# Kernel optimization log

Measured on AMD Instinct MI355X. Metric: run time of the kernel, lower is better.

The kernel has to match this reference:

```python
import jax, jax.numpy as jnp
import numpy as np

I, H, M, C, LOC, K = 512, 256, 80, 1024, 32, 31
C2 = C // 2
B, S, T = 32, 256, 800


def setup_inputs() -> dict:
    key = jax.random.key(0)
    ks = jax.random.split(key, 20)
    sc = 0.02
    return {
        "encodings": jax.random.normal(ks[0], (B, S, I), jnp.float32),
        "queries": jax.random.normal(ks[1], (B, T, H), jnp.float32),
        "outputs": jax.random.normal(ks[2], (B, T, M), jnp.float32),
        "mask": jnp.ones((B, S), jnp.float32),
        # GRUCell (PyTorch layout: gates ordered r, z, n)
        "w_ih": jax.random.normal(ks[3], (3 * C, I + H), jnp.float32) * sc,
        "w_hh": jax.random.normal(ks[4], (3 * C, C), jnp.float32) * sc,
        "b_ih": jax.random.normal(ks[5], (3 * C,), jnp.float32) * sc,
        "b_hh": jax.random.normal(ks[6], (3 * C,), jnp.float32) * sc,
        "w_q": jax.random.normal(ks[7], (C2, C), jnp.float32) * sc,        # proj_query
        "w_loc1": jax.random.normal(ks[8], (LOC, 1, K), jnp.float32) * sc, # Conv1d(1, loc, K)
        "w_loc2": jax.random.normal(ks[9], (C2, LOC), jnp.float32) * sc,   # Conv1d(loc, C2, 1)
        "w_k": jax.random.normal(ks[10], (C2, I), jnp.float32) * sc,       # proj_key
        "b_k": jax.random.normal(ks[11], (C2,), jnp.float32) * sc,
        "w_agg": jax.random.normal(ks[12], (C2,), jnp.float32) * sc,       # Conv1d(C2, 1, 1)
        "w_t1": jax.random.normal(ks[13], (C, I + C + M), jnp.float32) * sc,
        "b_t1": jax.random.normal(ks[14], (C,), jnp.float32) * sc,
        "w_t2": jax.random.normal(ks[15], (C,), jnp.float32) * sc,
    }


def _conv1d(x, w, pad):
    # x: [B, Cin, S], w: [Cout, Cin, K]
    return jax.lax.conv_general_dilated(
        x, w, window_strides=(1,), padding=[(pad, pad)],
        dimension_numbers=("NCH", "OIH", "NCH"))


def _aligner(encodings, queries, outputs, maskb,
             w_ih, w_hh, b_ih, b_hh, w_q, w_loc1, w_loc2, w_k, b_k,
             w_agg, w_t1, b_t1, w_t2):
    bsize, seqlen, _ = encodings.shape
    # key projection: [B, S, C2]
    key = encodings @ w_k.T + b_k
    h0 = jnp.zeros((bsize, C), encodings.dtype)
    align0 = jnp.full((bsize, seqlen), 1.0 / seqlen, encodings.dtype)
    alpha0 = jnp.zeros((bsize, seqlen), encodings.dtype).at[:, 0].set(1.0)
    trans0 = jnp.full((bsize, 1), 0.5, encodings.dtype)

    def step(carry, xt):
        h, align, trans, alpha = carry
        query, frame = xt  # [B,H], [B,M]
        prev = jnp.einsum("bsi,bs->bi", encodings, alpha)
        x = jnp.concatenate([query, prev], axis=-1)  # [B, H+I]
        gx = x @ w_ih.T + b_ih
        gh = h @ w_hh.T + b_hh
        xr, xz, xn = jnp.split(gx, 3, axis=-1)
        hr, hz, hn = jnp.split(gh, 3, axis=-1)
        r = jax.nn.sigmoid(xr + hr)
        z = jax.nn.sigmoid(xz + hz)
        n = jnp.tanh(xn + r * hn)
        h_new = (1.0 - z) * n + z * h  # GRUCell update
        # location features: [B,1,S] -> [B,LOC,S] -> [B,C2,S]
        loc = _conv1d(align[:, None, :], w_loc1, K // 2)
        loc = jnp.einsum("cl,bls->bcs", w_loc2, loc)
        score = loc + (h_new @ w_q.T)[..., None] + key.swapaxes(1, 2)  # [B,C2,S]
        energy = jnp.einsum("c,bcs->bs", w_agg, jnp.tanh(score))
        energy = jnp.where(maskb, -jnp.inf, energy)
        align_new = jax.nn.softmax(energy, axis=-1)
        shifted = jnp.pad(alpha, ((0, 0), (1, 0)))[:, :-1]  # F.pad(alpha, [1,-1])
        alpha_new = ((1.0 - trans) * alpha + trans * shifted + 1e-7) * align_new
        alpha_new = alpha_new / alpha_new.sum(axis=-1, keepdims=True)
        attend = jnp.einsum("bsi,bs->bi", encodings, alpha_new)
        t_in = jnp.concatenate([attend, frame, h_new], axis=-1)
        t = jax.nn.sigmoid(jnp.tanh(t_in @ w_t1.T + b_t1) @ w_t2[:, None])  # [B,1]
        return (h_new, align_new, t, alpha_new), alpha_new

    xs = (queries.swapaxes(0, 1), outputs.swapaxes(0, 1))
    _, alphas = jax.lax.scan(step, (h0, align0, trans0, alpha0), xs)
    return alphas.swapaxes(0, 1)  # [B, T, S]


def reference(encodings, queries, outputs, mask,
              w_ih, w_hh, b_ih, b_hh, w_q, w_loc1, w_loc2, w_k, b_k,
              w_agg, w_t1, b_t1, w_t2):
    maskb = ~(mask.astype(bool))
    return _aligner(encodings, queries, outputs, maskb,
                    w_ih, w_hh, b_ih, b_hh, w_q, w_loc1, w_loc2, w_k, b_k,
                    w_agg, w_t1, b_t1, w_t2)
```

## Files before the change

kernel.cpp:

```cpp
#include <hip/hip_runtime.h>
#include <cstdint>
#include <cstddef>


namespace cfg {
constexpr int NB = 32, NS = 256, NI = 512, NHq = 256, NM = 80;
constexpr int NC = 1024, NC2 = 512, NT = 800;
constexpr int NBLK = 256, NTHR = 512;

constexpr size_t OFF_KEYT  = 0;
constexpr size_t OFF_WKT   = OFF_KEYT + (size_t)NB * NS * NC2;
constexpr size_t OFF_PU    = OFF_WKT + (size_t)NI * NC2;
constexpr size_t OFF_H     = OFF_PU + (size_t)2 * NB * NI;
constexpr size_t OFF_H16   = OFF_H + (size_t)2 * NC * NB;
constexpr size_t OFF_E     = OFF_H16 + (size_t)NB * NC;
constexpr size_t OFF_W     = OFF_E + (size_t)2 * NB * NS;
constexpr size_t OFF_SE    = OFF_W + (size_t)2 * NB * NS;
constexpr size_t OFF_SW    = OFF_SE + 64;
constexpr size_t OFF_TPART = OFF_SW + 64;
constexpr size_t OFF_TRED  = OFF_TPART + (size_t)NBLK * NB;
constexpr size_t OFF_QBUF  = OFF_TRED + 32;
constexpr size_t OFF_BAR   = OFF_QBUF + (size_t)NB * NC2;
constexpr size_t OFF_Q16   = OFF_BAR + 4608;
constexpr size_t OFF_F16   = OFF_Q16 + (size_t)NT * NB * NHq / 2;
constexpr size_t OFF_WQ16  = OFF_F16 + (size_t)NT * NB * 128 / 2;
constexpr size_t WS_FLOATS = OFF_WQ16 + (size_t)NC2 * NC / 2;
}
using namespace cfg;

typedef __attribute__((ext_vector_type(8))) short short8;
typedef __attribute__((ext_vector_type(4))) float f32x4;

#define MF(a, b, c) __builtin_amdgcn_mfma_f32_16x16x32_bf16((a), (b), (c), 0, 0, 0)
#define LDSC(d, p) asm volatile("global_load_dwordx4 %0, %1, off sc0 sc1" : "=v"(d) : "v"(p))

__device__ __forceinline__ float ld_cg(const float* p) {
  return __hip_atomic_load(p, __ATOMIC_RELAXED, __HIP_MEMORY_SCOPE_AGENT);
}
__device__ __forceinline__ void st_cg(float* p, float v) {
  __hip_atomic_store(p, v, __ATOMIC_RELAXED, __HIP_MEMORY_SCOPE_AGENT);
}
__device__ __forceinline__ void st_cg_u16(unsigned short* p, unsigned short v) {
  asm volatile("global_store_short %0, %1, off sc0 sc1" :: "v"(p), "v"((unsigned)v) : "memory");
}

__device__ __forceinline__ void vw7(short8& a0, short8& a1, short8& a2, short8& a3,
                                    short8& a4, short8& a5, short8& a6) {
  asm volatile("s_waitcnt vmcnt(0)"
               : "+v"(a0), "+v"(a1), "+v"(a2), "+v"(a3), "+v"(a4), "+v"(a5), "+v"(a6));
}
__device__ __forceinline__ void vw8(short8& a0, short8& a1, short8& a2, short8& a3,
                                    short8& a4, short8& a5, short8& a6, short8& a7) {
  asm volatile("s_waitcnt vmcnt(0)"
               : "+v"(a0), "+v"(a1), "+v"(a2), "+v"(a3), "+v"(a4), "+v"(a5), "+v"(a6), "+v"(a7));
}
__device__ __forceinline__ void vw10(short8& a0, short8& a1, short8& a2, short8& a3, short8& a4,
                                     short8& a5, short8& a6, short8& a7, short8& a8, short8& a9) {
  asm volatile("s_waitcnt vmcnt(0)"
               : "+v"(a0), "+v"(a1), "+v"(a2), "+v"(a3), "+v"(a4), "+v"(a5), "+v"(a6),
                 "+v"(a7), "+v"(a8), "+v"(a9));
}
__device__ __forceinline__ void vw15(short8& a0, short8& a1, short8& a2, short8& a3, short8& a4,
                                     short8& a5, short8& a6, short8& a7, short8& a8, short8& a9,
                                     short8& aa, short8& ab2, short8& ac, short8& ad, short8& ae) {
  asm volatile("s_waitcnt vmcnt(0)"
               : "+v"(a0), "+v"(a1), "+v"(a2), "+v"(a3), "+v"(a4), "+v"(a5), "+v"(a6),
                 "+v"(a7), "+v"(a8), "+v"(a9), "+v"(aa), "+v"(ab2), "+v"(ac), "+v"(ad), "+v"(ae));
}
__device__ __forceinline__ void vw16f(f32x4& a0, f32x4& a1, f32x4& a2, f32x4& a3, f32x4& a4,
                                      f32x4& a5, f32x4& a6, f32x4& a7, f32x4& b0, f32x4& b1,
                                      f32x4& b2, f32x4& b3, f32x4& b4, f32x4& b5, f32x4& b6,
                                      f32x4& b7) {
  asm volatile("s_waitcnt vmcnt(0)"
               : "+v"(a0), "+v"(a1), "+v"(a2), "+v"(a3), "+v"(a4), "+v"(a5), "+v"(a6), "+v"(a7),
                 "+v"(b0), "+v"(b1), "+v"(b2), "+v"(b3), "+v"(b4), "+v"(b5), "+v"(b6), "+v"(b7));
}

__device__ __forceinline__ float frcp(float x) {
#if __has_builtin(__builtin_amdgcn_rcpf)
  return __builtin_amdgcn_rcpf(x);
#else
  return 1.f / x;
#endif
}
__device__ __forceinline__ float fsig(float x) { return frcp(1.f + __expf(-x)); }
__device__ __forceinline__ float ftanh(float x) {
  const float e = __expf(2.f * x);
  return 1.f - 2.f * frcp(e + 1.f);
}
__device__ __forceinline__ short f2bf(float f) {
  unsigned u = __float_as_uint(f);
  u += 0x7FFFu + ((u >> 16) & 1u);
  return (short)(u >> 16);
}
__device__ __forceinline__ float bf2f(short s) {
  return __uint_as_float(((unsigned)(unsigned short)s) << 16);
}
__device__ __forceinline__ short8 cvt8(f32x4 lo, f32x4 hi) {
  short8 a;
  a[0] = f2bf(lo[0]); a[1] = f2bf(lo[1]); a[2] = f2bf(lo[2]); a[3] = f2bf(lo[3]);
  a[4] = f2bf(hi[0]); a[5] = f2bf(hi[1]); a[6] = f2bf(hi[2]); a[7] = f2bf(hi[3]);
  return a;
}

__device__ __forceinline__ void gbarrier(unsigned* root, unsigned* flags, unsigned& ph) {
  ++ph;
  asm volatile("s_waitcnt vmcnt(0)" ::: "memory");
  __syncthreads();
  if (blockIdx.x == 0) {
    const int t = threadIdx.x;
    if (t > 0 && t < 256) {
      while (__hip_atomic_load(&flags[t * 16], __ATOMIC_RELAXED, __HIP_MEMORY_SCOPE_AGENT) < ph)
        __builtin_amdgcn_s_sleep(1);
    }
    __syncthreads();
    if (t == 0)
      __hip_atomic_store(root, ph, __ATOMIC_RELAXED, __HIP_MEMORY_SCOPE_AGENT);
  } else {
    if (threadIdx.x == 0) {
      __hip_atomic_store(&flags[blockIdx.x * 16], ph, __ATOMIC_RELAXED, __HIP_MEMORY_SCOPE_AGENT);
      while (__hip_atomic_load(root, __ATOMIC_RELAXED, __HIP_MEMORY_SCOPE_AGENT) < ph)
        __builtin_amdgcn_s_sleep(1);
    }
  }
  __syncthreads();
}

__device__ __forceinline__ float wcat_val(const float* __restrict__ w_ih,
                                          const float* __restrict__ w_hh,
                                          const float* __restrict__ w_t1,
                                          int kind, int c, int k) {
  if (kind < 3) {
    const int gr = kind * NC + c;
    if (k < 768) return w_ih[(size_t)gr * 768 + k];
    if (k < 1792) return w_hh[(size_t)gr * NC + (k - 768)];
    return 0.f;
  }
  if (k >= 256 && k < 768) return w_t1[(size_t)c * 1616 + (k - 256)];
  if (k >= 768 && k < 1792) return w_t1[(size_t)c * 1616 + 592 + (k - 768)];
  if (k >= 1792 && k < 1872) return w_t1[(size_t)c * 1616 + 512 + (k - 1792)];
  return 0.f;
}

__global__ void k_init(const float* __restrict__ enc, const float* __restrict__ queries,
                       const float* __restrict__ outputs, const float* __restrict__ w_k,
                       const float* __restrict__ w_q, float* __restrict__ ws) {
  const size_t t0 = (size_t)blockIdx.x * blockDim.x + threadIdx.x;
  const size_t gs = (size_t)gridDim.x * blockDim.x;
  for (size_t x = t0; x < (size_t)NI * NC2; x += gs) {
    const int i = (int)(x / NC2), c2 = (int)(x % NC2);
    ws[OFF_WKT + x] = w_k[(size_t)c2 * NI + i];
  }
  for (size_t x = t0; x < (size_t)NB * NI; x += gs) {
    const int b = (int)(x / NI), i = (int)(x % NI);
    ws[OFF_PU + x] = 0.f;
    ws[OFF_PU + (size_t)NB * NI + b * NI + i] = enc[(size_t)b * NS * NI + i];
  }
  for (size_t x = t0; x < (size_t)2 * NC * NB; x += gs) ws[OFF_H + x] = 0.f;
  for (size_t x = t0; x < (size_t)NB * NC; x += gs) ws[OFF_H16 + x] = 0.f;
  for (size_t x = t0; x < (size_t)NB * NS; x += gs) {
    ws[OFF_E + x] = 0.f;
    ws[OFF_E + (size_t)NB * NS + x] = 1.f;
    ws[OFF_W + x] = 0.f;
    ws[OFF_W + (size_t)NB * NS + x] = ((x & (NS - 1)) == 0) ? 1.f : 0.f;
  }
  for (size_t x = t0; x < (size_t)NB; x += gs) {
    ws[OFF_SE + x] = 0.f; ws[OFF_SE + NB + x] = (float)NS;
    ws[OFF_SW + x] = 0.f; ws[OFF_SW + NB + x] = 1.f;
    ws[OFF_TRED + x] = 0.f;
  }
  unsigned* bar = (unsigned*)(ws + OFF_BAR);
  for (size_t x = t0; x < 4608; x += gs) bar[x] = 0u;
  unsigned short* Q16 = (unsigned short*)(ws + OFF_Q16);
  for (size_t x = t0; x < (size_t)NT * NB * NHq; x += gs) {
    const int k = (int)(x & (NHq - 1));
    const int b = (int)((x >> 8) & (NB - 1));
    const int t = (int)(x >> 13);
    Q16[x] = (unsigned short)f2bf(queries[((size_t)b * NT + t) * NHq + k]);
  }
  unsigned short* F16 = (unsigned short*)(ws + OFF_F16);
  for (size_t x = t0; x < (size_t)NT * NB * 128; x += gs) {
    const int k = (int)(x & 127);
    const int b = (int)((x >> 7) & (NB - 1));
    const int t = (int)(x >> 12);
    F16[x] = (k < NM) ? (unsigned short)f2bf(outputs[((size_t)b * NT + t) * NM + k]) : 0;
  }
  unsigned short* WQ16 = (unsigned short*)(ws + OFF_WQ16);
  for (size_t x = t0; x < (size_t)NC2 * NC; x += gs)
    WQ16[x] = (unsigned short)f2bf(w_q[x]);
}

__global__ __launch_bounds__(NTHR) void k_key(const float* __restrict__ enc,
                                              const float* __restrict__ b_k,
                                              float* __restrict__ ws) {
  __shared__ float encl[4 * NI];
  const int bid = blockIdx.x, tid = threadIdx.x;
  const int b = bid >> 3, s0 = (bid & 7) * 32;
  const float* wkT = ws + OFF_WKT;
  float* keyT = ws + OFF_KEYT;
  const float bk = b_k[tid];
  for (int q = 0; q < 8; ++q) {
    const int sb = s0 + q * 4;
    for (int x = tid; x < 4 * NI; x += NTHR) {
      const int ss = x >> 9, i = x & (NI - 1);
      encl[x] = enc[((size_t)(b * NS + sb + ss)) * NI + i];
    }
    __syncthreads();
    float a0 = bk, a1 = bk, a2 = bk, a3 = bk;
    for (int i = 0; i < NI; ++i) {
      const float wv = wkT[(size_t)i * NC2 + tid];
      a0 += wv * encl[i];           a1 += wv * encl[NI + i];
      a2 += wv * encl[2 * NI + i];  a3 += wv * encl[3 * NI + i];
    }
    keyT[((size_t)(b * NS + sb + 0)) * NC2 + tid] = a0;
    keyT[((size_t)(b * NS + sb + 1)) * NC2 + tid] = a1;
    keyT[((size_t)(b * NS + sb + 2)) * NC2 + tid] = a2;
    keyT[((size_t)(b * NS + sb + 3)) * NC2 + tid] = a3;
    __syncthreads();
  }
}

__global__ __launch_bounds__(NTHR, 2) void k_main(
    const float* __restrict__ enc, const float* __restrict__ mask,
    const float* __restrict__ w_ih, const float* __restrict__ w_hh,
    const float* __restrict__ b_ih, const float* __restrict__ b_hh,
    const float* __restrict__ w_loc1, const float* __restrict__ w_loc2,
    const float* __restrict__ w_agg, const float* __restrict__ w_t1,
    const float* __restrict__ b_t1, const float* __restrict__ w_t2,
    float* ws, float* __restrict__ out) {
  const int bid = blockIdx.x, tid = threadIdx.x;
  float* const keyT = ws + OFF_KEYT;
  float* const PU = ws + OFF_PU;
  float* const HB = ws + OFF_H;
  unsigned short* const HB16 = (unsigned short*)(ws + OFF_H16);
  float* const EB = ws + OFF_E;
  float* const WBUF = ws + OFF_W;
  float* const SEB = ws + OFF_SE;
  float* const SWB = ws + OFF_SW;
  float* const TPART = ws + OFF_TPART;
  float* const TRED = ws + OFF_TRED;
  float* const QBUF = ws + OFF_QBUF;
  unsigned* const root = (unsigned*)(ws + OFF_BAR);
  unsigned* const flags = root + 16;
  const unsigned short* const Q16 = (const unsigned short*)(ws + OFF_Q16);
  const unsigned short* const F16 = (const unsigned short*)(ws + OFF_F16);
  const unsigned short* const WQ16 = (const unsigned short*)(ws + OFF_WQ16);

  __shared__ float Cred[2 * 5 * 4 * 64];
  __shared__ float gout2[5 * 4 * 32];
  __shared__ float swinv_l[32];
  __shared__ float tredl[128];
  __shared__ float alignl[72];
  __shared__ float wl2[34];
  __shared__ float qbl[520];
  __shared__ float Epart[32 * 9];
  __shared__ float wstash[32];
  __shared__ float scal[4];

  const int lane = tid & 63, wv = tid >> 6;
  const int m2 = wv >> 2, k4 = wv & 3;
  const int kg = lane >> 4;
  const int ab = m2 * 16 + (lane & 15);
  const int cs = bid * 4;
  const int pb_b = bid >> 3, pb_s0 = (bid & 7) * 32;
  const int col = lane & 15, quad = lane >> 4;
  unsigned ph = 0;

  short8 wreg[16];
  {
    const int n = lane & 15;
    const int kind = n >> 2, ch = cs + (n & 3);
#pragma unroll
    for (int si = 0; si < 16; ++si) {
      int s = (k4 == 0) ? (si < 8 ? si : (si < 15 ? 16 + si : -1))
            : (k4 == 1) ? 8 + si
            : (k4 == 2) ? (si < 15 ? 31 + si : -1)
                        : (si < 14 ? 46 + si : -1);
      short8 w = {0, 0, 0, 0, 0, 0, 0, 0};
      if (s >= 0) {
        const int k0 = s * 32 + kg * 8;
#pragma unroll
        for (int jj = 0; jj < 8; ++jj)
          w[jj] = f2bf(wcat_val(w_ih, w_hh, w_t1, kind, ch, k0 + jj));
      }
      wreg[si] = w;
    }
  }
  short8 wcA[4];
  unsigned keylo[4][2], keyhi[4][2];
  f32x4 wagr[4];
#pragma unroll
  for (int t = 0; t < 4; ++t) {
    const int mt = 4 * wv + t;
    short8 wfr;
#pragma unroll
    for (int jj = 0; jj < 8; ++jj) {
      const int k = quad * 8 + jj;
      float s = 0.f;
      if (k < 31) {
        const int c2 = mt * 16 + col;
        for (int l = 0; l < 32; ++l) s += w_loc2[c2 * 32 + l] * w_loc1[l * 31 + k];
      }
      wfr[jj] = f2bf(s);
    }
    wcA[t] = wfr;
    const int c2r = mt * 16 + quad * 4;
#pragma unroll
    for (int r = 0; r < 4; ++r) wagr[t][r] = w_agg[c2r + r];
#pragma unroll
    for (int nt = 0; nt < 2; ++nt) {
      const float* kp = &keyT[((size_t)(pb_b * NS + pb_s0 + nt * 16 + col)) * NC2 + c2r];
      keylo[t][nt] = ((unsigned)(unsigned short)f2bf(kp[0])) |
                     (((unsigned)(unsigned short)f2bf(kp[1])) << 16);
      keyhi[t][nt] = ((unsigned)(unsigned short)f2bf(kp[2])) |
                     (((unsigned)(unsigned short)f2bf(kp[3])) << 16);
    }
  }
  if (tid >= 62 && tid < 72) alignl[tid] = 0.f;
  __syncthreads();

  for (int j = 0; j < NT; ++j) {
    const int p = j & 1;
    const float* pu_prev = PU + (size_t)(1 - p) * NB * NI;
    float* pu_cur = PU + (size_t)p * NB * NI;
    const float* h_prev = HB + (size_t)(1 - p) * NC * NB;
    float* h_cur = HB + (size_t)p * NC * NB;
    const unsigned short* hb16_prev = HB16 + (size_t)(1 - p) * NB * NC;
    unsigned short* hb16_cur = HB16 + (size_t)p * NB * NC;
    const float* e_prev = EB + (size_t)(1 - p) * NB * NS;
    float* e_cur = EB + (size_t)p * NB * NS;
    const float* w_prev = WBUF + (size_t)(1 - p) * NB * NS;
    float* w_cur = WBUF + (size_t)p * NB * NS;
    const float* se_prev = SEB + (size_t)(1 - p) * NB;
    float* se_cur = SEB + (size_t)p * NB;
    const float* sw_prev = SWB + (size_t)(1 - p) * NB;
    float* sw_cur = SWB + (size_t)p * NB;

    if (tid < 64) st_cg(&pu_cur[bid * 64 + tid], 0.f);
    if (bid == 0 && tid < NB) st_cg(&se_cur[tid], 0.f);
    if (bid == 1 && tid < NB) st_cg(&sw_cur[tid], 0.f);
    if (tid < NB) swinv_l[tid] = 1.f / ld_cg(&sw_prev[tid]);
    __syncthreads();

    if (j >= 1 && bid < NB && tid < NS)
      out[((size_t)bid * NT + (j - 1)) * NS + tid] = ld_cg(&w_prev[bid * NS + tid]) * swinv_l[bid];

    f32x4 accA = {0.f, 0.f, 0.f, 0.f}, accB = {0.f, 0.f, 0.f, 0.f};
    if (k4 == 0) {
      const unsigned short* qp = Q16 + ((size_t)j * NB + ab) * NHq + kg * 8;
      const unsigned short* hp = hb16_prev + (size_t)ab * NC + kg * 8;
      short8 h0, h1, h2, h3, h4, h5, h6;
      LDSC(h0, hp);        LDSC(h1, hp + 32);   LDSC(h2, hp + 64);  LDSC(h3, hp + 96);
      LDSC(h4, hp + 128);  LDSC(h5, hp + 160);  LDSC(h6, hp + 192);
      const short8 q0 = *(const short8*)(qp);
      const short8 q1 = *(const short8*)(qp + 32);
      const short8 q2 = *(const short8*)(qp + 64);
      const short8 q3 = *(const short8*)(qp + 96);
      const short8 q4 = *(const short8*)(qp + 128);
      const short8 q5 = *(const short8*)(qp + 160);
      const short8 q6 = *(const short8*)(qp + 192);
      const short8 q7 = *(const short8*)(qp + 224);
      vw7(h0, h1, h2, h3, h4, h5, h6);
      accA = MF(q0, wreg[0], accA); accA = MF(q1, wreg[1], accA);
      accA = MF(q2, wreg[2], accA); accA = MF(q3, wreg[3], accA);
      accA = MF(q4, wreg[4], accA); accA = MF(q5, wreg[5], accA);
      accA = MF(q6, wreg[6], accA); accA = MF(q7, wreg[7], accA);
      accB = MF(h0, wreg[8], accB);  accB = MF(h1, wreg[9], accB);
      accB = MF(h2, wreg[10], accB); accB = MF(h3, wreg[11], accB);
      accB = MF(h4, wreg[12], accB); accB = MF(h5, wreg[13], accB);
      accB = MF(h6, wreg[14], accB);
    } else if (k4 == 1) {
      const float* pp = pu_prev + (size_t)ab * NI + kg * 8;
#pragma unroll
      for (int rd = 0; rd < 2; ++rd) {
        const float* pb = pp + rd * 256;
        f32x4 a0, a1, a2, a3, a4, a5, a6, a7, b0, b1, b2, b3, b4, b5, b6, b7;
        LDSC(a0, pb);        LDSC(b0, pb + 4);
        LDSC(a1, pb + 32);   LDSC(b1, pb + 36);
        LDSC(a2, pb + 64);   LDSC(b2, pb + 68);
        LDSC(a3, pb + 96);   LDSC(b3, pb + 100);
        LDSC(a4, pb + 128);  LDSC(b4, pb + 132);
        LDSC(a5, pb + 160);  LDSC(b5, pb + 164);
        LDSC(a6, pb + 192);  LDSC(b6, pb + 196);
        LDSC(a7, pb + 224);  LDSC(b7, pb + 228);
        vw16f(a0, a1, a2, a3, a4, a5, a6, a7, b0, b1, b2, b3, b4, b5, b6, b7);
        const int w0 = rd * 8;
        accA = MF(cvt8(a0, b0), wreg[w0 + 0], accA);
        accA = MF(cvt8(a1, b1), wreg[w0 + 1], accA);
        accA = MF(cvt8(a2, b2), wreg[w0 + 2], accA);
        accA = MF(cvt8(a3, b3), wreg[w0 + 3], accA);
        accA = MF(cvt8(a4, b4), wreg[w0 + 4], accA);
        accA = MF(cvt8(a5, b5), wreg[w0 + 5], accA);
        accA = MF(cvt8(a6, b6), wreg[w0 + 6], accA);
        accA = MF(cvt8(a7, b7), wreg[w0 + 7], accA);
      }
    } else if (k4 == 2) {
      const unsigned short* hp = hb16_prev + (size_t)ab * NC + kg * 8 + 224;
      short8 h0, h1, h2, h3, h4, h5, h6, h7, h8, h9, ha, hb2, hc, hd, he;
      LDSC(h0, hp);        LDSC(h1, hp + 32);  LDSC(h2, hp + 64);  LDSC(h3, hp + 96);
      LDSC(h4, hp + 128);  LDSC(h5, hp + 160); LDSC(h6, hp + 192); LDSC(h7, hp + 224);
      LDSC(h8, hp + 256);  LDSC(h9, hp + 288); LDSC(ha, hp + 320); LDSC(hb2, hp + 352);
      LDSC(hc, hp + 384);  LDSC(hd, hp + 416); LDSC(he, hp + 448);
      vw15(h0, h1, h2, h3, h4, h5, h6, h7, h8, h9, ha, hb2, hc, hd, he);
      accA = MF(h0, wreg[0], accA);  accA = MF(h1, wreg[1], accA);
      accA = MF(h2, wreg[2], accA);  accA = MF(h3, wreg[3], accA);
      accA = MF(h4, wreg[4], accA);  accA = MF(h5, wreg[5], accA);
      accA = MF(h6, wreg[6], accA);  accA = MF(h7, wreg[7], accA);
      accA = MF(h8, wreg[8], accA);  accA = MF(h9, wreg[9], accA);
      accA = MF(ha, wreg[10], accA); accA = MF(hb2, wreg[11], accA);
      accA = MF(hc, wreg[12], accA); accA = MF(hd, wreg[13], accA);
      accA = MF(he, wreg[14], accA);
    } else {
      const unsigned short* hp = hb16_prev + (size_t)ab * NC + kg * 8 + 704;
      short8 h0, h1, h2, h3, h4, h5, h6, h7, h8, h9;
      LDSC(h0, hp);        LDSC(h1, hp + 32);  LDSC(h2, hp + 64);  LDSC(h3, hp + 96);
      LDSC(h4, hp + 128);  LDSC(h5, hp + 160); LDSC(h6, hp + 192); LDSC(h7, hp + 224);
      LDSC(h8, hp + 256);  LDSC(h9, hp + 288);
      short8 f0 = {0,0,0,0,0,0,0,0}, f1 = f0, f2 = f0, f3 = f0;
      if (j > 0) {
        const unsigned short* fp = F16 + ((size_t)(j - 1) * NB + ab) * 128 + kg * 8;
        f0 = *(const short8*)(fp);
        f1 = *(const short8*)(fp + 32);
        f2 = *(const short8*)(fp + 64);
        f3 = *(const short8*)(fp + 96);
      }
      vw10(h0, h1, h2, h3, h4, h5, h6, h7, h8, h9);
      accA = MF(h0, wreg[0], accA); accA = MF(h1, wreg[1], accA);
      accA = MF(h2, wreg[2], accA); accA = MF(h3, wreg[3], accA);
      accA = MF(h4, wreg[4], accA); accA = MF(h5, wreg[5], accA);
      accA = MF(h6, wreg[6], accA); accA = MF(h7, wreg[7], accA);
      accA = MF(h8, wreg[8], accA); accA = MF(h9, wreg[9], accA);
      accA = MF(f0, wreg[10], accA); accA = MF(f1, wreg[11], accA);
      accA = MF(f2, wreg[12], accA); accA = MF(f3, wreg[13], accA);
    }
    {
      auto cidx = [](int m, int sg, int r, int l) { return ((m * 5 + sg) * 4 + r) * 64 + l; };
      if (k4 == 0) {
#pragma unroll
        for (int r = 0; r < 4; ++r) {
          Cred[cidx(m2, 0, r, lane)] = accA[r];
          Cred[cidx(m2, 1, r, lane)] = accB[r];
        }
      } else {
        const int sg = 1 + k4;
#pragma unroll
        for (int r = 0; r < 4; ++r) Cred[cidx(m2, sg, r, lane)] = accA[r];
      }
    }
    __syncthreads();
    {
      const int n = tid & 15, b = tid >> 4;
      const int m2r = b >> 4, bm = b & 15, l = (bm >> 2) * 16 + n, r = bm & 3;
      auto cidx = [](int m, int sg, int rr, int ll) { return ((m * 5 + sg) * 4 + rr) * 64 + ll; };
      const float s0 = Cred[cidx(m2r, 0, r, l)];
      const float sB = Cred[cidx(m2r, 1, r, l)];
      const float s1 = Cred[cidx(m2r, 2, r, l)];
      const float s2 = sB + Cred[cidx(m2r, 3, r, l)] + Cred[cidx(m2r, 4, r, l)];
      const float swv = swinv_l[b];
      const int kind = n >> 2, c4o = n & 3;
      if (kind == 2) {
        gout2[2 * 128 + c4o * 32 + b] = s0 + swv * s1;
        gout2[3 * 128 + c4o * 32 + b] = s2;
      } else {
        const int slot = (kind == 3) ? 4 : kind;
        gout2[slot * 128 + c4o * 32 + b] = s0 + swv * s1 + s2;
      }
    }
    __syncthreads();
    if (tid < 128) {
      const int c4o = tid >> 5, b = tid & 31, c = cs + c4o;
      const float xr = gout2[0 * 128 + c4o * 32 + b] + b_ih[c] + b_hh[c];
      const float xz = gout2[1 * 128 + c4o * 32 + b] + b_ih[NC + c] + b_hh[NC + c];
      const float xn = gout2[2 * 128 + c4o * 32 + b] + b_ih[2 * NC + c];
      const float hn = gout2[3 * 128 + c4o * 32 + b] + b_hh[2 * NC + c];
      const float tp = gout2[4 * 128 + c4o * 32 + b];
      const float r = fsig(xr), z = fsig(xz);
      const float nn = ftanh(xn + r * hn);
      const float hnew = (1.f - z) * nn + z * h_prev[c * 32 + b];
      h_cur[c * 32 + b] = hnew;
      st_cg_u16(&hb16_cur[(size_t)b * NC + c], (unsigned short)f2bf(hnew));
      tredl[c4o * 32 + b] = w_t2[c] * ftanh(tp + b_t1[c]);
    }
    __syncthreads();
    if (tid < NB)
      st_cg(&TPART[bid * NB + tid],
            tredl[tid] + tredl[32 + tid] + tredl[64 + tid] + tredl[96 + tid]);
    gbarrier(root, flags, ph);

    if (bid < 32) {
      f32x4 qacc = {0.f, 0.f, 0.f, 0.f};
      const unsigned short* hb = HB16 + (size_t)p * NB * NC + (size_t)ab * NC + kg * 8;
      short8 g0, g1, g2, g3, g4, g5, g6, g7;
      LDSC(g0, hb + (k4 * 8 + 0) * 32); LDSC(g1, hb + (k4 * 8 + 1) * 32);
      LDSC(g2, hb + (k4 * 8 + 2) * 32); LDSC(g3, hb + (k4 * 8 + 3) * 32);
      LDSC(g4, hb + (k4 * 8 + 4) * 32); LDSC(g5, hb + (k4 * 8 + 5) * 32);
      LDSC(g6, hb + (k4 * 8 + 6) * 32); LDSC(g7, hb + (k4 * 8 + 7) * 32);
      const int jq = bid * 16 + col;
      const unsigned short* wp = WQ16 + (size_t)jq * NC + k4 * 8 * 32 + kg * 8;
      vw8(g0, g1, g2, g3, g4, g5, g6, g7);
      qacc = MF(g0, *(const short8*)(wp), qacc);
      qacc = MF(g1, *(const short8*)(wp + 32), qacc);
      qacc = MF(g2, *(const short8*)(wp + 64), qacc);
      qacc = MF(g3, *(const short8*)(wp + 96), qacc);
      qacc = MF(g4, *(const short8*)(wp + 128), qacc);
      qacc = MF(g5, *(const short8*)(wp + 160), qacc);
      qacc = MF(g6, *(const short8*)(wp + 192), qacc);
      qacc = MF(g7, *(const short8*)(wp + 224), qacc);
#pragma unroll
      for (int r = 0; r < 4; ++r) Cred[((m2 * 4 + k4) * 4 + r) * 64 + lane] = qacc[r];
      __syncthreads();
      {
        const int col2 = tid & 15, b2 = tid >> 4;
        const int m2r = b2 >> 4, bm = b2 & 15, l = (bm >> 2) * 16 + col2, r = bm & 3;
        float s = 0.f;
#pragma unroll
        for (int kk = 0; kk < 4; ++kk) s += Cred[((m2r * 4 + kk) * 4 + r) * 64 + l];
        st_cg(&QBUF[(size_t)b2 * NC2 + bid * 16 + col2], s);
      }
    } else if (bid >= 64 && bid < 96) {
      const int b2 = bid - 64;
      float v = (tid < NBLK) ? ld_cg(&TPART[tid * NB + b2]) : 0.f;
#pragma unroll
      for (int off = 32; off > 0; off >>= 1) v += __shfl_down(v, off);
      if (lane == 0) Cred[wv] = v;
      __syncthreads();
      if (tid == 0) {
        float s = 0.f;
#pragma unroll
        for (int w8 = 0; w8 < 8; ++w8) s += Cred[w8];
        st_cg(&TRED[b2], s);
      }
    }
    gbarrier(root, flags, ph);

    {
      const int b = pb_b, s0v = pb_s0;
      if (tid == 0) {
        scal[0] = ld_cg(&se_prev[b]);
        scal[1] = ld_cg(&sw_prev[b]);
        scal[2] = ld_cg(&TRED[b]);
      }
      qbl[tid] = ld_cg(&QBUF[(size_t)b * NC2 + tid]);
      if (tid < 62) {
        const int sp = s0v + tid - 15;
        alignl[tid] = (sp >= 0 && sp < NS) ? ld_cg(&e_prev[b * NS + sp]) : 0.f;
      }
      if (tid >= 64 && tid < 97) {
        const int i2 = tid - 64, sp = s0v + i2 - 1;
        wl2[i2] = (sp >= 0 && sp < NS) ? ld_cg(&w_prev[b * NS + sp]) : 0.f;
      }
      __syncthreads();
      const float invSE = 1.f / scal[0];
      const float invSW = 1.f / scal[1];
      const float tr = (j == 0) ? 0.5f : fsig(scal[2]);
      short8 bfr[2];
#pragma unroll
      for (int nt = 0; nt < 2; ++nt) {
        const int base = nt * 16 + col + quad * 8;
        short8 bv;
#pragma unroll
        for (int jj = 0; jj < 8; ++jj) bv[jj] = f2bf(alignl[base + jj] * invSE);
        bfr[nt] = bv;
      }
#pragma unroll
      for (int nt = 0; nt < 2; ++nt) {
        float pe = 0.f;
#pragma unroll
        for (int t = 0; t < 4; ++t) {
          const int c2b = (4 * wv + t) * 16 + quad * 4;
          f32x4 acc;
          acc[0] = qbl[c2b + 0] + __uint_as_float(keylo[t][nt] << 16);
          acc[1] = qbl[c2b + 1] + __uint_as_float(keylo[t][nt] & 0xffff0000u);
          acc[2] = qbl[c2b + 2] + __uint_as_float(keyhi[t][nt] << 16);
          acc[3] = qbl[c2b + 3] + __uint_as_float(keyhi[t][nt] & 0xffff0000u);
          acc = MF(wcA[t], bfr[nt], acc);
          pe += wagr[t][0] * ftanh(acc[0]);
          pe += wagr[t][1] * ftanh(acc[1]);
          pe += wagr[t][2] * ftanh(acc[2]);
          pe += wagr[t][3] * ftanh(acc[3]);
        }
        pe += __shfl_xor(pe, 16);
        pe += __shfl_xor(pe, 32);
        if (lane < 16) Epart[(nt * 16 + col) * 9 + wv] = pe;
      }
      __syncthreads();
      if (tid < 32) {
        const int sl = tid, s = s0v + sl;
        float Ev = 0.f;
#pragma unroll
        for (int w8 = 0; w8 < 8; ++w8) Ev += Epart[sl * 9 + w8];
        const float ev = (mask[b * NS + s] != 0.f) ? __expf(Ev) : 0.f;
        const float csv = ((1.f - tr) * wl2[sl + 1] + tr * wl2[sl]) * invSW + 1e-7f;
        const float wvv = csv * ev;
        st_cg(&e_cur[b * NS + s], ev);
        st_cg(&w_cur[b * NS + s], wvv);
        wstash[sl] = wvv;
        float se = ev, sw2 = wvv;
#pragma unroll
        for (int off = 16; off > 0; off >>= 1) {
          se += __shfl_down(se, off, 32);
          sw2 += __shfl_down(sw2, off, 32);
        }
        if (sl == 0) { atomicAdd(&se_cur[b], se); atomicAdd(&sw_cur[b], sw2); }
      }
      __syncthreads();
      {
        float acc = 0.f;
        const float* encb = enc + ((size_t)(b * NS + s0v)) * NI + tid;
#pragma unroll 8
        for (int ss = 0; ss < 32; ++ss) acc += wstash[ss] * encb[(size_t)ss * NI];
        atomicAdd(&pu_cur[(size_t)b * NI + tid], acc);
      }
    }
    gbarrier(root, flags, ph);
  }

  if (bid < NB && tid < NS) {
    const float invSW = 1.f / ld_cg(&SWB[NB + bid]);
    out[((size_t)bid * NT + (NT - 1)) * NS + tid] =
        ld_cg(&WBUF[(size_t)NB * NS + bid * NS + tid]) * invSW;
  }
}

extern "C" void kernel_launch(void* const* d_in, const int* in_sizes, int n_in,
                              void* d_out, int out_size, void* d_ws, size_t ws_size,
                              hipStream_t stream) {
  const float* enc     = (const float*)d_in[0];
  const float* queries = (const float*)d_in[1];
  const float* outputs = (const float*)d_in[2];
  const float* mask    = (const float*)d_in[3];
  const float* w_ih    = (const float*)d_in[4];
  const float* w_hh    = (const float*)d_in[5];
  const float* b_ih    = (const float*)d_in[6];
  const float* b_hh    = (const float*)d_in[7];
  const float* w_q     = (const float*)d_in[8];
  const float* w_loc1  = (const float*)d_in[9];
  const float* w_loc2  = (const float*)d_in[10];
  const float* w_k     = (const float*)d_in[11];
  const float* b_k     = (const float*)d_in[12];
  const float* w_agg   = (const float*)d_in[13];
  const float* w_t1    = (const float*)d_in[14];
  const float* b_t1    = (const float*)d_in[15];
  const float* w_t2    = (const float*)d_in[16];
  float* ws = (float*)d_ws;
  float* out = (float*)d_out;
  (void)in_sizes; (void)n_in; (void)out_size; (void)ws_size;

  k_init<<<dim3(1024), dim3(256), 0, stream>>>(enc, queries, outputs, w_k, w_q, ws);
  k_key<<<dim3(NBLK), dim3(NTHR), 0, stream>>>(enc, b_k, ws);
  k_main<<<dim3(NBLK), dim3(NTHR), 0, stream>>>(enc, mask, w_ih, w_hh, b_ih, b_hh,
                                                w_loc1, w_loc2, w_agg, w_t1,
                                                b_t1, w_t2, ws, out);
}
```

Baseline: 21.28 ms.

## Replace second grid barrier with per-block flags and hoist location-conv MFMA earlier

Replaces the second global barrier of each timestep with per-producer flag counters: the blocks that compute query projections and the transition reduction publish a step counter, and consumers spin only on those 64 flags. The location-convolution MFMA and key-term setup, which depend only on previous-step data, are moved ahead of the GRU reduction so they overlap with other work. The query term is added afterward before tanh. This trades a full barrier for targeted polling and keeps extra accumulators live in registers, which raises register pressure.

```diff
diff --git a/kernel.cpp b/kernel.cpp
--- a/kernel.cpp
+++ b/kernel.cpp
@@ -242,6 +242,7 @@
   float* const QBUF = ws + OFF_QBUF;
   unsigned* const root = (unsigned*)(ws + OFF_BAR);
   unsigned* const flags = root + 16;
+  unsigned* const qflags = root + 4112;
   const unsigned short* const Q16 = (const unsigned short*)(ws + OFF_Q16);
   const unsigned short* const F16 = (const unsigned short*)(ws + OFF_F16);
   const unsigned short* const WQ16 = (const unsigned short*)(ws + OFF_WQ16);
@@ -336,10 +337,21 @@
     const float* sw_prev = SWB + (size_t)(1 - p) * NB;
     float* sw_cur = SWB + (size_t)p * NB;
 
+    f32x4 bacc[2][4];
+
     if (tid < 64) st_cg(&pu_cur[bid * 64 + tid], 0.f);
     if (bid == 0 && tid < NB) st_cg(&se_cur[tid], 0.f);
     if (bid == 1 && tid < NB) st_cg(&sw_cur[tid], 0.f);
     if (tid < NB) swinv_l[tid] = 1.f / ld_cg(&sw_prev[tid]);
+    if (tid == 0) scal[0] = ld_cg(&se_prev[pb_b]);
+    if (tid < 62) {
+      const int sp = pb_s0 + tid - 15;
+      alignl[tid] = (sp >= 0 && sp < NS) ? ld_cg(&e_prev[pb_b * NS + sp]) : 0.f;
+    }
+    if (tid >= 64 && tid < 97) {
+      const int i2 = tid - 64, sp = pb_s0 + i2 - 1;
+      wl2[i2] = (sp >= 0 && sp < NS) ? ld_cg(&w_prev[pb_b * NS + sp]) : 0.f;
+    }
     __syncthreads();
 
     if (j >= 1 && bid < NB && tid < NS)
@@ -447,6 +459,25 @@
         for (int r = 0; r < 4; ++r) Cred[cidx(m2, sg, r, lane)] = accA[r];
       }
     }
+    {
+      const float invSE = 1.f / scal[0];
+#pragma unroll
+      for (int nt = 0; nt < 2; ++nt) {
+        const int base = nt * 16 + col + quad * 8;
+        short8 bv;
+#pragma unroll
+        for (int jj = 0; jj < 8; ++jj) bv[jj] = f2bf(alignl[base + jj] * invSE);
+#pragma unroll
+        for (int t = 0; t < 4; ++t) {
+          f32x4 acc;
+          acc[0] = __uint_as_float(keylo[t][nt] << 16);
+          acc[1] = __uint_as_float(keylo[t][nt] & 0xffff0000u);
+          acc[2] = __uint_as_float(keyhi[t][nt] << 16);
+          acc[3] = __uint_as_float(keyhi[t][nt] & 0xffff0000u);
+          bacc[nt][t] = MF(wcA[t], bv, acc);
+        }
+      }
+    }
     __syncthreads();
     {
       const int n = tid & 15, b = tid >> 4;
@@ -489,7 +520,7 @@
 
     if (bid < 32) {
       f32x4 qacc = {0.f, 0.f, 0.f, 0.f};
-      const unsigned short* hb = HB16 + (size_t)p * NB * NC + (size_t)ab * NC + kg * 8;
+      const unsigned short* hb = hb16_cur + (size_t)ab * NC + kg * 8;
       short8 g0, g1, g2, g3, g4, g5, g6, g7;
       LDSC(g0, hb + (k4 * 8 + 0) * 32); LDSC(g1, hb + (k4 * 8 + 1) * 32);
       LDSC(g2, hb + (k4 * 8 + 2) * 32); LDSC(g3, hb + (k4 * 8 + 3) * 32);
@@ -517,6 +548,11 @@
         for (int kk = 0; kk < 4; ++kk) s += Cred[((m2r * 4 + kk) * 4 + r) * 64 + l];
         st_cg(&QBUF[(size_t)b2 * NC2 + bid * 16 + col2], s);
       }
+      asm volatile("s_waitcnt vmcnt(0)" ::: "memory");
+      __syncthreads();
+      if (tid == 0)
+        __hip_atomic_store(&qflags[bid * 4], (unsigned)(j + 1),
+                           __ATOMIC_RELAXED, __HIP_MEMORY_SCOPE_AGENT);
     } else if (bid >= 64 && bid < 96) {
       const int b2 = bid - 64;
       float v = (tid < NBLK) ? ld_cg(&TPART[tid * NB + b2]) : 0.f;
@@ -529,55 +565,37 @@
 #pragma unroll
         for (int w8 = 0; w8 < 8; ++w8) s += Cred[w8];
         st_cg(&TRED[b2], s);
-      }
-    }
-    gbarrier(root, flags, ph);
+        asm volatile("s_waitcnt vmcnt(0)" ::: "memory");
+        __hip_atomic_store(&qflags[(32 + b2) * 4], (unsigned)(j + 1),
+                           __ATOMIC_RELAXED, __HIP_MEMORY_SCOPE_AGENT);
+      }
+    }
 
     {
       const int b = pb_b, s0v = pb_s0;
-      if (tid == 0) {
-        scal[0] = ld_cg(&se_prev[b]);
-        scal[1] = ld_cg(&sw_prev[b]);
-        scal[2] = ld_cg(&TRED[b]);
-      }
+      if (tid < 64) {
+        const unsigned tgt = (unsigned)(j + 1);
+        while (__hip_atomic_load(&qflags[tid * 4], __ATOMIC_RELAXED,
+                                 __HIP_MEMORY_SCOPE_AGENT) < tgt)
+          __builtin_amdgcn_s_sleep(2);
+      }
+      __syncthreads();
       qbl[tid] = ld_cg(&QBUF[(size_t)b * NC2 + tid]);
-      if (tid < 62) {
-        const int sp = s0v + tid - 15;
-        alignl[tid] = (sp >= 0 && sp < NS) ? ld_cg(&e_prev[b * NS + sp]) : 0.f;
-      }
-      if (tid >= 64 && tid < 97) {
-        const int i2 = tid - 64, sp = s0v + i2 - 1;
-        wl2[i2] = (sp >= 0 && sp < NS) ? ld_cg(&w_prev[b * NS + sp]) : 0.f;
-      }
+      if (tid == 0) scal[2] = ld_cg(&TRED[b]);
       __syncthreads();
-      const float invSE = 1.f / scal[0];
-      const float invSW = 1.f / scal[1];
+      const float invSW = swinv_l[b];
       const float tr = (j == 0) ? 0.5f : fsig(scal[2]);
-      short8 bfr[2];
-#pragma unroll
-      for (int nt = 0; nt < 2; ++nt) {
-        const int base = nt * 16 + col + quad * 8;
-        short8 bv;
-#pragma unroll
-        for (int jj = 0; jj < 8; ++jj) bv[jj] = f2bf(alignl[base + jj] * invSE);
-        bfr[nt] = bv;
-      }
 #pragma unroll
       for (int nt = 0; nt < 2; ++nt) {
         float pe = 0.f;
 #pragma unroll
         for (int t = 0; t < 4; ++t) {
           const int c2b = (4 * wv + t) * 16 + quad * 4;
-          f32x4 acc;
-          acc[0] = qbl[c2b + 0] + __uint_as_float(keylo[t][nt] << 16);
-          acc[1] = qbl[c2b + 1] + __uint_as_float(keylo[t][nt] & 0xffff0000u);
-          acc[2] = qbl[c2b + 2] + __uint_as_float(keyhi[t][nt] << 16);
-          acc[3] = qbl[c2b + 3] + __uint_as_float(keyhi[t][nt] & 0xffff0000u);
-          acc = MF(wcA[t], bfr[nt], acc);
-          pe += wagr[t][0] * ftanh(acc[0]);
-          pe += wagr[t][1] * ftanh(acc[1]);
-          pe += wagr[t][2] * ftanh(acc[2]);
-          pe += wagr[t][3] * ftanh(acc[3]);
+          const f32x4 av = bacc[nt][t];
+          pe += wagr[t][0] * ftanh(av[0] + qbl[c2b + 0]);
+          pe += wagr[t][1] * ftanh(av[1] + qbl[c2b + 1]);
+          pe += wagr[t][2] * ftanh(av[2] + qbl[c2b + 2]);
+          pe += wagr[t][3] * ftanh(av[3] + qbl[c2b + 3]);
         }
         pe += __shfl_xor(pe, 16);
         pe += __shfl_xor(pe, 32);
```

New measurement: 22.37 ms. 1.05x slower.
